# Optimization experiments

Hardware: AMD Instinct MI355X
Metric: run time of the kernel (lower is better)

## Reference

```python
import math
import jax, jax.numpy as jnp
import numpy as np

T, C, NH = 2048, 1024, 16
HD = C // NH


def setup_inputs() -> dict:
    key = jax.random.key(0)
    ks = jax.random.split(key, 5)
    return {
        "x": jax.random.normal(ks[0], (T, C), dtype=jnp.float32),
        "w_attn": jax.random.normal(ks[1], (3 * C, C), dtype=jnp.float32) * (1.0 / math.sqrt(C)),
        "b_attn": jax.random.normal(ks[2], (3 * C,), dtype=jnp.float32) * 0.02,
        "w_proj": jax.random.normal(ks[3], (C, C), dtype=jnp.float32) * (1.0 / math.sqrt(C)),
        "b_proj": jax.random.normal(ks[4], (C,), dtype=jnp.float32) * 0.02,
    }


def reference(x, w_attn, b_attn, w_proj, b_proj):
    t, c = x.shape
    # qkv projection: eqx Linear computes W @ x + b, vmapped over T
    qkv = x @ w_attn.T + b_attn  # (T, 3C)
    q, k, v = jnp.split(qkv, 3, axis=1)  # each (T, C)
    # (T, NH, HD) -> (NH, T, HD)
    q = jnp.swapaxes(q.reshape(t, NH, HD), 0, 1)
    k = jnp.swapaxes(k.reshape(t, NH, HD), 0, 1)
    v = jnp.swapaxes(v.reshape(t, NH, HD), 0, 1)
    att = jnp.einsum('hqd,hkd->hqk', q, k) / math.sqrt(HD)  # (NH, T, T)
    causal = jnp.tril(jnp.ones((t, t), dtype=bool))
    att = jnp.where(causal[None, :, :], att, -jnp.inf)
    att = jax.nn.softmax(att, axis=-1)
    y = jnp.matmul(att, v)  # (NH, T, HD)
    # Faithful to source: swapaxes(1,2) on (NH, T, HD) -> (NH, HD, T), then reshape
    y = jnp.swapaxes(y, 1, 2).reshape(t, c)
    return y @ w_proj.T + b_proj
```

## Files before the change

### kernel.cpp

```cpp
#include <hip/hip_runtime.h>
#include <hip/hip_bf16.h>
#include <stdint.h>

typedef __bf16 bf16;
typedef __bf16 bf16x8 __attribute__((ext_vector_type(8)));
typedef __bf16 bf16x4 __attribute__((ext_vector_type(4)));
typedef float floatx4 __attribute__((ext_vector_type(4)));

#define T_DIM 2048
#define C_DIM 1024
#define NH    16
#define HD    64

__device__ __forceinline__ void gload_lds16(const void* g, void* l) {
    __builtin_amdgcn_global_load_lds(
        (__attribute__((address_space(1))) void*)(g),
        (__attribute__((address_space(3))) void*)(l),
        16, 0, 0);
}

#define MFMA16(a, b, c) __builtin_amdgcn_mfma_f32_16x16x32_bf16(a, b, c, 0, 0, 0)

__global__ __launch_bounds__(256) void cvt_all(
    const float* __restrict__ x, const float* __restrict__ wa,
    const float* __restrict__ wp,
    bf16* __restrict__ xb, bf16* __restrict__ wab, bf16* __restrict__ wpb)
{
    const int i = blockIdx.x * 256 + threadIdx.x;
    const float* src; bf16* dst; int off;
    if (i < 262144)      { src = x;  dst = xb;  off = i; }
    else if (i < 655360) { src = wa; dst = wab; off = i - 262144; }
    else                 { src = wp; dst = wpb; off = i - 655360; }
    const float4 a = ((const float4*)src)[off * 2];
    const float4 b = ((const float4*)src)[off * 2 + 1];
    bf16x8 o;
    o[0] = (bf16)a.x; o[1] = (bf16)a.y; o[2] = (bf16)a.z; o[3] = (bf16)a.w;
    o[4] = (bf16)b.x; o[5] = (bf16)b.y; o[6] = (bf16)b.z; o[7] = (bf16)b.w;
    *(bf16x8*)(dst + (size_t)off * 8) = o;
}

template<int MODE, int TN>
__global__ __launch_bounds__(256) void csa_gemm_bt(
    const bf16* __restrict__ A, const bf16* __restrict__ B,
    const float* __restrict__ bias,
    void* __restrict__ out0v, bf16* __restrict__ out1, bf16* __restrict__ out2)
{
    constexpr int K = 1024;
    constexpr int MT = (TN == 128) ? 4 : 2;
    __shared__ __align__(16) bf16 sA[128 * 32];
    __shared__ __align__(16) bf16 sB[TN * 32];

    const int tid  = threadIdx.x;
    const int lane = tid & 63;
    const int wid  = tid >> 6;
    const int rowbase = (TN == 128) ? (wid & 1) * 64 : wid * 32;
    const int colbase = (TN == 128) ? (wid >> 1) * 64 : 0;
    const int tileM = blockIdx.x * 128;
    const int tileN = blockIdx.y * TN;

    const int r0 = tid >> 2;
    const int c0 = (tid & 3) * 8;
    const long aBase = (long)(tileM + r0) * K + c0;
    const long bBase = (long)(tileN + r0) * K + c0;

    const int fr   = lane & 15;
    const int quad = lane >> 4;
    const int fc   = quad * 8;

    floatx4 acc[MT][4];
#pragma unroll
    for (int i = 0; i < MT; i++)
#pragma unroll
        for (int j = 0; j < 4; j++) acc[i][j] = (floatx4){0.f, 0.f, 0.f, 0.f};

    for (int k0 = 0; k0 < K; k0 += 32) {
        __syncthreads();
        gload_lds16(A + aBase + k0,                 sA + tid * 8);
        gload_lds16(A + aBase + (long)64 * K + k0,  sA + 2048 + tid * 8);
        gload_lds16(B + bBase + k0,                 sB + tid * 8);
        if (TN == 128)
            gload_lds16(B + bBase + (long)64 * K + k0, sB + 2048 + tid * 8);
        __syncthreads();

        bf16x8 af[MT], bfr[4];
#pragma unroll
        for (int mt = 0; mt < MT; mt++)
            af[mt] = *(const bf16x8*)(sA + (rowbase + mt * 16 + fr) * 32 + fc);
#pragma unroll
        for (int nt = 0; nt < 4; nt++)
            bfr[nt] = *(const bf16x8*)(sB + (colbase + nt * 16 + fr) * 32 + fc);
#pragma unroll
        for (int mt = 0; mt < MT; mt++)
#pragma unroll
            for (int nt = 0; nt < 4; nt++)
                acc[mt][nt] = MFMA16(af[mt], bfr[nt], acc[mt][nt]);
    }

#pragma unroll
    for (int mt = 0; mt < MT; mt++) {
#pragma unroll
        for (int nt = 0; nt < 4; nt++) {
            const int gn = tileN + colbase + nt * 16 + fr;
            const float bv = bias[gn];
            const int gmb = tileM + rowbase + mt * 16 + quad * 4;
            if (MODE == 0) {
                const int which = gn >> 10;
                const int w2 = gn & 1023;
                const int hh = w2 >> 6, d = w2 & 63;
                if (which == 2) {
                    bf16x4 pk;
#pragma unroll
                    for (int r = 0; r < 4; r++) pk[r] = (bf16)(acc[mt][nt][r] + bv);
                    *(bf16x4*)(out2 + ((long)(hh * HD + d) << 11) + gmb) = pk;
                } else {
                    bf16* dst = (which == 0) ? (bf16*)out0v : out1;
#pragma unroll
                    for (int r = 0; r < 4; r++)
                        dst[((long)hh * T_DIM + gmb + r) * HD + d] =
                            (bf16)(acc[mt][nt][r] + bv);
                }
            } else {
#pragma unroll
                for (int r = 0; r < 4; r++)
                    ((float*)out0v)[(long)(gmb + r) * C_DIM + gn] =
                        acc[mt][nt][r] + bv;
            }
        }
    }
}

__global__ __launch_bounds__(256) void csa_attn_chunk(
    const bf16* __restrict__ Qh, const bf16* __restrict__ Kh,
    const bf16* __restrict__ Vth, float* __restrict__ Opart,
    float* __restrict__ lpart, bf16* __restrict__ YY)
{
    __shared__ __align__(16) bf16 sK[2][64 * 64];
    __shared__ __align__(16) bf16 sV[2][64 * 64];
    __shared__ __align__(16) bf16 sP[4][16 * 64];

    const int qt = blockIdx.x;
    const int h  = blockIdx.y;
    const int c  = blockIdx.z;
    const int nk = qt + 1;
    const int kt0 = c * 8;
    if (kt0 >= nk) return;
    const int ktend = (kt0 + 8 < nk) ? kt0 + 8 : nk;

    const int tid  = threadIdx.x;
    const int lane = tid & 63;
    const int wid  = tid >> 6;
    const int fr   = lane & 15;
    const int quad = lane >> 4;
    const int f7   = fr & 7;
    const int q0   = qt * 64;
    const int qg   = q0 + wid * 16 + fr;

    const bf16* qrow = Qh + ((long)h * T_DIM + qg) * HD;
    const bf16x8 qf0 = *(const bf16x8*)(qrow + quad * 8);
    const bf16x8 qf1 = *(const bf16x8*)(qrow + quad * 8 + 32);

    const int rb   = tid >> 3;
    const int cswz = (tid & 7) ^ (rb & 7);

    auto stage = [&](int b, int k0) {
        gload_lds16(Kh + ((long)(h * T_DIM + k0 + rb) << 6) + cswz * 8,
                    &sK[b][0] + tid * 8);
        gload_lds16(Kh + ((long)(h * T_DIM + k0 + rb + 32) << 6) + cswz * 8,
                    &sK[b][0] + 2048 + tid * 8);
        gload_lds16(Vth + ((long)(h * HD + rb) << 11) + k0 + cswz * 8,
                    &sV[b][0] + tid * 8);
        gload_lds16(Vth + ((long)(h * HD + rb + 32) << 11) + k0 + cswz * 8,
                    &sV[b][0] + 2048 + tid * 8);
    };

    stage(0, kt0 * 64);

    float l_i = 0.f;
    floatx4 o_acc[4];
#pragma unroll
    for (int d4 = 0; d4 < 4; d4++) o_acc[d4] = (floatx4){0.f, 0.f, 0.f, 0.f};

    for (int kt = kt0; kt < ktend; ++kt) {
        const int it = kt - kt0;
        __syncthreads();
        if (kt + 1 < ktend) stage((it + 1) & 1, (kt + 1) * 64);
        const bf16* K_ = &sK[it & 1][0];
        const bf16* V_ = &sV[it & 1][0];
        const int k0 = kt * 64;
        const bool diag = (kt == qt);

        float p[4][4];
#pragma unroll
        for (int nt = 0; nt < 4; nt++) {
            const bf16* kr = K_ + (nt * 16 + fr) * 64;
            const bf16x8 ka0 = *(const bf16x8*)(kr + (quad ^ f7) * 8);
            const bf16x8 ka1 = *(const bf16x8*)(kr + ((quad + 4) ^ f7) * 8);
            floatx4 z = (floatx4){0.f, 0.f, 0.f, 0.f};
            z = MFMA16(ka0, qf0, z);
            z = MFMA16(ka1, qf1, z);
            const int kgb = k0 + nt * 16 + quad * 4;
#pragma unroll
            for (int r = 0; r < 4; r++) {
                const float e = __builtin_amdgcn_exp2f(z[r] * 0.1803368801f);
                p[nt][r] = (!diag || (kgb + r <= qg)) ? e : 0.f;
            }
        }

        float s = 0.f;
#pragma unroll
        for (int nt = 0; nt < 4; nt++)
#pragma unroll
            for (int r = 0; r < 4; r++) s += p[nt][r];
        s += __shfl_xor(s, 16);
        s += __shfl_xor(s, 32);
        l_i += s;

        bf16* pw = &sP[wid][0];
#pragma unroll
        for (int nt = 0; nt < 4; nt++) {
            bf16x4 pk;
#pragma unroll
            for (int r = 0; r < 4; r++) pk[r] = (bf16)p[nt][r];
            *(bf16x4*)(pw + fr * 64 +
                       (((2 * nt + (quad >> 1)) ^ f7) * 8) + (quad & 1) * 4) = pk;
        }
        asm volatile("s_waitcnt lgkmcnt(0)" ::: "memory");
        const bf16x8 pa0 = *(const bf16x8*)(pw + fr * 64 + (quad ^ f7) * 8);
        const bf16x8 pa1 = *(const bf16x8*)(pw + fr * 64 + ((quad + 4) ^ f7) * 8);

#pragma unroll
        for (int d4 = 0; d4 < 4; d4++) {
            const bf16* vr = V_ + (d4 * 16 + fr) * 64;
            const bf16x8 vb0 = *(const bf16x8*)(vr + (quad ^ f7) * 8);
            const bf16x8 vb1 = *(const bf16x8*)(vr + ((quad + 4) ^ f7) * 8);
            o_acc[d4] = MFMA16(pa0, vb0, o_acc[d4]);
            o_acc[d4] = MFMA16(pa1, vb1, o_acc[d4]);
        }
    }

    if (kt0 == 0 && ktend == nk) {
        const float inv_self = 1.f / l_i;
        float inv[4];
#pragma unroll
        for (int r = 0; r < 4; r++) inv[r] = __shfl(inv_self, quad * 4 + r);
#pragma unroll
        for (int r = 0; r < 4; r++) {
            const int q = q0 + wid * 16 + quad * 4 + r;
            const int rq = q >> 10, cq = q & 1023;
#pragma unroll
            for (int d4 = 0; d4 < 4; d4++) {
                const int d = d4 * 16 + fr;
                YY[(long)(h * 128 + 2 * d + rq) * 1024 + cq] =
                    (bf16)(o_acc[d4][r] * inv[r]);
            }
        }
    } else {
        const long obase = ((long)((h * 32 + qt) * 4 + c)) * 4096;
#pragma unroll
        for (int d4 = 0; d4 < 4; d4++)
#pragma unroll
            for (int r = 0; r < 4; r++)
                Opart[obase + (wid * 16 + quad * 4 + r) * 64 + d4 * 16 + fr] =
                    o_acc[d4][r];
        if (quad == 0)
            lpart[((h * 32 + qt) * 4 + c) * 64 + wid * 16 + fr] = l_i;
    }
}

__global__ __launch_bounds__(256) void csa_combine(
    const float* __restrict__ Opart, const float* __restrict__ lpart,
    bf16* __restrict__ YY)
{
    const int qt = blockIdx.x + 8;
    const int h  = blockIdx.y;
    const int nc = (qt >> 3) + 1;
    const int t  = threadIdx.x;
    const int q  = t >> 2;
    const int d0 = (t & 3) * 16;

    const long obase = ((long)((h * 32 + qt) * 4)) * 4096 + q * 64 + d0;
    const int  lbase = (h * 32 + qt) * 4 * 64 + q;

    float4 acc[4] = {};
    float lq = 0.f;
    for (int c = 0; c < nc; c++) {
        const float4* src = (const float4*)(Opart + obase + (long)c * 4096);
#pragma unroll
        for (int j = 0; j < 4; j++) {
            const float4 v = src[j];
            acc[j].x += v.x; acc[j].y += v.y; acc[j].z += v.z; acc[j].w += v.w;
        }
        lq += lpart[lbase + c * 64];
    }
    const float inv = 1.f / lq;
    const int qglob = qt * 64 + q;
    const int rq = qglob >> 10, cq = qglob & 1023;
#pragma unroll
    for (int j = 0; j < 4; j++) {
        const float vv[4] = {acc[j].x, acc[j].y, acc[j].z, acc[j].w};
#pragma unroll
        for (int k = 0; k < 4; k++) {
            const int d = d0 + j * 4 + k;
            YY[(long)(h * 128 + 2 * d + rq) * 1024 + cq] = (bf16)(vv[k] * inv);
        }
    }
}

extern "C" void kernel_launch(void* const* d_in, const int* in_sizes, int n_in,
                              void* d_out, int out_size, void* d_ws, size_t ws_size,
                              hipStream_t stream) {
    (void)in_sizes; (void)n_in; (void)out_size; (void)ws_size;
    const float* x      = (const float*)d_in[0];
    const float* w_attn = (const float*)d_in[1];
    const float* b_attn = (const float*)d_in[2];
    const float* w_proj = (const float*)d_in[3];
    const float* b_proj = (const float*)d_in[4];

    bf16* xb  = (bf16*)d_ws;
    bf16* wab = xb  + (size_t)T_DIM * C_DIM;
    bf16* wpb = wab + (size_t)3 * C_DIM * C_DIM;
    bf16* Q   = wpb + (size_t)C_DIM * C_DIM;
    bf16* Kp  = Q   + (size_t)NH * T_DIM * HD;
    bf16* Vt  = Kp  + (size_t)NH * T_DIM * HD;
    bf16* YY  = Vt  + (size_t)NH * T_DIM * HD;
    float* Opart = (float*)(YY + (size_t)T_DIM * C_DIM);
    float* lpart = Opart + (size_t)16 * 32 * 4 * 4096;

    cvt_all<<<3072, 256, 0, stream>>>(x, w_attn, w_proj, xb, wab, wpb);

    csa_gemm_bt<0, 128><<<dim3(16, 24), 256, 0, stream>>>(xb, wab, b_attn, Q, Kp, Vt);
    csa_attn_chunk<<<dim3(32, NH, 4), 256, 0, stream>>>(Q, Kp, Vt, Opart, lpart, YY);
    csa_combine<<<dim3(24, NH), 256, 0, stream>>>(Opart, lpart, YY);
    csa_gemm_bt<1, 64><<<dim3(16, 16), 256, 0, stream>>>(YY, wpb, b_proj, d_out, nullptr, nullptr);
}
```

Measured before the change: 157.0 us.

## Enlarge attention query tile to 128 rows and launch heaviest tiles first

The attention kernel now gives each wave 32 query rows (two 16-row halves) instead of 16, so every K/V tile staged in shared memory serves twice as many queries. This halves K/V load traffic per query and doubles MFMA work per barrier. The grid is reordered so the longest causal query tiles are scheduled first, and the combine kernel and partial buffers are resized to match. The cost is higher register pressure, larger shared P buffers and fewer blocks, which can lower occupancy.

After: 162.0 us. 1.03x slower.

```diff
diff --git a/kernel.cpp b/kernel.cpp
--- a/kernel.cpp
+++ b/kernel.cpp
@@ -136,12 +136,12 @@
 {
     __shared__ __align__(16) bf16 sK[2][64 * 64];
     __shared__ __align__(16) bf16 sV[2][64 * 64];
-    __shared__ __align__(16) bf16 sP[4][16 * 64];
-
-    const int qt = blockIdx.x;
+    __shared__ __align__(16) bf16 sP[4][32 * 64];
+
+    const int c  = blockIdx.x;
     const int h  = blockIdx.y;
-    const int c  = blockIdx.z;
-    const int nk = qt + 1;
+    const int qt = 15 - (int)blockIdx.z;
+    const int nk = 2 * qt + 2;
     const int kt0 = c * 8;
     if (kt0 >= nk) return;
     const int ktend = (kt0 + 8 < nk) ? kt0 + 8 : nk;
@@ -152,12 +152,15 @@
     const int fr   = lane & 15;
     const int quad = lane >> 4;
     const int f7   = fr & 7;
-    const int q0   = qt * 64;
-    const int qg   = q0 + wid * 16 + fr;
-
-    const bf16* qrow = Qh + ((long)h * T_DIM + qg) * HD;
-    const bf16x8 qf0 = *(const bf16x8*)(qrow + quad * 8);
-    const bf16x8 qf1 = *(const bf16x8*)(qrow + quad * 8 + 32);
+    const int qw   = qt * 128 + wid * 32;
+
+    bf16x8 qf[2][2];
+#pragma unroll
+    for (int half = 0; half < 2; half++) {
+        const bf16* qrow = Qh + ((long)h * T_DIM + qw + half * 16 + fr) * HD;
+        qf[half][0] = *(const bf16x8*)(qrow + quad * 8);
+        qf[half][1] = *(const bf16x8*)(qrow + quad * 8 + 32);
+    }
 
     const int rb   = tid >> 3;
     const int cswz = (tid & 7) ^ (rb & 7);
@@ -175,10 +178,12 @@
 
     stage(0, kt0 * 64);
 
-    float l_i = 0.f;
-    floatx4 o_acc[4];
-#pragma unroll
-    for (int d4 = 0; d4 < 4; d4++) o_acc[d4] = (floatx4){0.f, 0.f, 0.f, 0.f};
+    float l_i[2] = {0.f, 0.f};
+    floatx4 o_acc[2][4];
+#pragma unroll
+    for (int half = 0; half < 2; half++)
+#pragma unroll
+        for (int d4 = 0; d4 < 4; d4++) o_acc[half][d4] = (floatx4){0.f, 0.f, 0.f, 0.f};
 
     for (int kt = kt0; kt < ktend; ++kt) {
         const int it = kt - kt0;
@@ -187,83 +192,108 @@
         const bf16* K_ = &sK[it & 1][0];
         const bf16* V_ = &sV[it & 1][0];
         const int k0 = kt * 64;
-        const bool diag = (kt == qt);
-
-        float p[4][4];
+        const bool need_mask = (kt >= 2 * qt);
+
+        float p[2][4][4];
 #pragma unroll
         for (int nt = 0; nt < 4; nt++) {
             const bf16* kr = K_ + (nt * 16 + fr) * 64;
             const bf16x8 ka0 = *(const bf16x8*)(kr + (quad ^ f7) * 8);
             const bf16x8 ka1 = *(const bf16x8*)(kr + ((quad + 4) ^ f7) * 8);
-            floatx4 z = (floatx4){0.f, 0.f, 0.f, 0.f};
-            z = MFMA16(ka0, qf0, z);
-            z = MFMA16(ka1, qf1, z);
             const int kgb = k0 + nt * 16 + quad * 4;
 #pragma unroll
-            for (int r = 0; r < 4; r++) {
-                const float e = __builtin_amdgcn_exp2f(z[r] * 0.1803368801f);
-                p[nt][r] = (!diag || (kgb + r <= qg)) ? e : 0.f;
-            }
-        }
-
-        float s = 0.f;
-#pragma unroll
-        for (int nt = 0; nt < 4; nt++)
-#pragma unroll
-            for (int r = 0; r < 4; r++) s += p[nt][r];
-        s += __shfl_xor(s, 16);
-        s += __shfl_xor(s, 32);
-        l_i += s;
+            for (int half = 0; half < 2; half++) {
+                floatx4 z = (floatx4){0.f, 0.f, 0.f, 0.f};
+                z = MFMA16(ka0, qf[half][0], z);
+                z = MFMA16(ka1, qf[half][1], z);
+                const int qg = qw + half * 16 + fr;
+#pragma unroll
+                for (int r = 0; r < 4; r++) {
+                    const float e = __builtin_amdgcn_exp2f(z[r] * 0.1803368801f);
+                    p[half][nt][r] = (!need_mask || (kgb + r <= qg)) ? e : 0.f;
+                }
+            }
+        }
+
+#pragma unroll
+        for (int half = 0; half < 2; half++) {
+            float s = 0.f;
+#pragma unroll
+            for (int nt = 0; nt < 4; nt++)
+#pragma unroll
+                for (int r = 0; r < 4; r++) s += p[half][nt][r];
+            s += __shfl_xor(s, 16);
+            s += __shfl_xor(s, 32);
+            l_i[half] += s;
+        }
 
         bf16* pw = &sP[wid][0];
 #pragma unroll
-        for (int nt = 0; nt < 4; nt++) {
-            bf16x4 pk;
-#pragma unroll
-            for (int r = 0; r < 4; r++) pk[r] = (bf16)p[nt][r];
-            *(bf16x4*)(pw + fr * 64 +
-                       (((2 * nt + (quad >> 1)) ^ f7) * 8) + (quad & 1) * 4) = pk;
-        }
+        for (int half = 0; half < 2; half++)
+#pragma unroll
+            for (int nt = 0; nt < 4; nt++) {
+                bf16x4 pk;
+#pragma unroll
+                for (int r = 0; r < 4; r++) pk[r] = (bf16)p[half][nt][r];
+                *(bf16x4*)(pw + (half * 16 + fr) * 64 +
+                           (((2 * nt + (quad >> 1)) ^ f7) * 8) + (quad & 1) * 4) = pk;
+            }
         asm volatile("s_waitcnt lgkmcnt(0)" ::: "memory");
-        const bf16x8 pa0 = *(const bf16x8*)(pw + fr * 64 + (quad ^ f7) * 8);
-        const bf16x8 pa1 = *(const bf16x8*)(pw + fr * 64 + ((quad + 4) ^ f7) * 8);
+        bf16x8 pa[2][2];
+#pragma unroll
+        for (int half = 0; half < 2; half++) {
+            pa[half][0] = *(const bf16x8*)(pw + (half * 16 + fr) * 64 + (quad ^ f7) * 8);
+            pa[half][1] = *(const bf16x8*)(pw + (half * 16 + fr) * 64 + ((quad + 4) ^ f7) * 8);
+        }
 
 #pragma unroll
         for (int d4 = 0; d4 < 4; d4++) {
             const bf16* vr = V_ + (d4 * 16 + fr) * 64;
             const bf16x8 vb0 = *(const bf16x8*)(vr + (quad ^ f7) * 8);
             const bf16x8 vb1 = *(const bf16x8*)(vr + ((quad + 4) ^ f7) * 8);
-            o_acc[d4] = MFMA16(pa0, vb0, o_acc[d4]);
-            o_acc[d4] = MFMA16(pa1, vb1, o_acc[d4]);
+#pragma unroll
+            for (int half = 0; half < 2; half++) {
+                o_acc[half][d4] = MFMA16(pa[half][0], vb0, o_acc[half][d4]);
+                o_acc[half][d4] = MFMA16(pa[half][1], vb1, o_acc[half][d4]);
+            }
         }
     }
 
     if (kt0 == 0 && ktend == nk) {
-        const float inv_self = 1.f / l_i;
-        float inv[4];
-#pragma unroll
-        for (int r = 0; r < 4; r++) inv[r] = __shfl(inv_self, quad * 4 + r);
-#pragma unroll
-        for (int r = 0; r < 4; r++) {
-            const int q = q0 + wid * 16 + quad * 4 + r;
-            const int rq = q >> 10, cq = q & 1023;
-#pragma unroll
-            for (int d4 = 0; d4 < 4; d4++) {
-                const int d = d4 * 16 + fr;
-                YY[(long)(h * 128 + 2 * d + rq) * 1024 + cq] =
-                    (bf16)(o_acc[d4][r] * inv[r]);
+#pragma unroll
+        for (int half = 0; half < 2; half++) {
+            const float inv_self = 1.f / l_i[half];
+            float inv[4];
+#pragma unroll
+            for (int r = 0; r < 4; r++) inv[r] = __shfl(inv_self, quad * 4 + r);
+#pragma unroll
+            for (int r = 0; r < 4; r++) {
+                const int q = qw + half * 16 + quad * 4 + r;
+                const int rq = q >> 10, cq = q & 1023;
+#pragma unroll
+                for (int d4 = 0; d4 < 4; d4++) {
+                    const int d = d4 * 16 + fr;
+                    YY[(long)(h * 128 + 2 * d + rq) * 1024 + cq] =
+                        (bf16)(o_acc[half][d4][r] * inv[r]);
+                }
             }
         }
     } else {
-        const long obase = ((long)((h * 32 + qt) * 4 + c)) * 4096;
-#pragma unroll
-        for (int d4 = 0; d4 < 4; d4++)
-#pragma unroll
-            for (int r = 0; r < 4; r++)
-                Opart[obase + (wid * 16 + quad * 4 + r) * 64 + d4 * 16 + fr] =
-                    o_acc[d4][r];
-        if (quad == 0)
-            lpart[((h * 32 + qt) * 4 + c) * 64 + wid * 16 + fr] = l_i;
+        const long obase = ((long)((h * 16 + qt) * 4 + c)) * 8192;
+#pragma unroll
+        for (int half = 0; half < 2; half++)
+#pragma unroll
+            for (int d4 = 0; d4 < 4; d4++)
+#pragma unroll
+                for (int r = 0; r < 4; r++)
+                    Opart[obase + (wid * 32 + half * 16 + quad * 4 + r) * 64 +
+                          d4 * 16 + fr] = o_acc[half][d4][r];
+        if (quad == 0) {
+#pragma unroll
+            for (int half = 0; half < 2; half++)
+                lpart[((h * 16 + qt) * 4 + c) * 128 + wid * 32 + half * 16 + fr] =
+                    l_i[half];
+        }
     }
 }
 
@@ -271,32 +301,32 @@
     const float* __restrict__ Opart, const float* __restrict__ lpart,
     bf16* __restrict__ YY)
 {
-    const int qt = blockIdx.x + 8;
+    const int qt = blockIdx.x + 4;
     const int h  = blockIdx.y;
-    const int nc = (qt >> 3) + 1;
+    const int nc = (2 * qt + 2 + 7) >> 3;
     const int t  = threadIdx.x;
-    const int q  = t >> 2;
-    const int d0 = (t & 3) * 16;
-
-    const long obase = ((long)((h * 32 + qt) * 4)) * 4096 + q * 64 + d0;
-    const int  lbase = (h * 32 + qt) * 4 * 64 + q;
-
-    float4 acc[4] = {};
+    const int row = t >> 1;
+    const int d0  = (t & 1) * 32;
+
+    const long obase = ((long)((h * 16 + qt) * 4)) * 8192 + row * 64 + d0;
+    const int  lbase = (h * 16 + qt) * 4 * 128 + row;
+
+    float4 acc[8] = {};
     float lq = 0.f;
     for (int c = 0; c < nc; c++) {
-        const float4* src = (const float4*)(Opart + obase + (long)c * 4096);
-#pragma unroll
-        for (int j = 0; j < 4; j++) {
+        const float4* src = (const float4*)(Opart + obase + (long)c * 8192);
+#pragma unroll
+        for (int j = 0; j < 8; j++) {
             const float4 v = src[j];
             acc[j].x += v.x; acc[j].y += v.y; acc[j].z += v.z; acc[j].w += v.w;
         }
-        lq += lpart[lbase + c * 64];
+        lq += lpart[lbase + c * 128];
     }
     const float inv = 1.f / lq;
-    const int qglob = qt * 64 + q;
+    const int qglob = qt * 128 + row;
     const int rq = qglob >> 10, cq = qglob & 1023;
 #pragma unroll
-    for (int j = 0; j < 4; j++) {
+    for (int j = 0; j < 8; j++) {
         const float vv[4] = {acc[j].x, acc[j].y, acc[j].z, acc[j].w};
 #pragma unroll
         for (int k = 0; k < 4; k++) {
@@ -324,12 +354,12 @@
     bf16* Vt  = Kp  + (size_t)NH * T_DIM * HD;
     bf16* YY  = Vt  + (size_t)NH * T_DIM * HD;
     float* Opart = (float*)(YY + (size_t)T_DIM * C_DIM);
-    float* lpart = Opart + (size_t)16 * 32 * 4 * 4096;
+    float* lpart = Opart + (size_t)16 * 16 * 4 * 8192;
 
     cvt_all<<<3072, 256, 0, stream>>>(x, w_attn, w_proj, xb, wab, wpb);
 
     csa_gemm_bt<0, 128><<<dim3(16, 24), 256, 0, stream>>>(xb, wab, b_attn, Q, Kp, Vt);
-    csa_attn_chunk<<<dim3(32, NH, 4), 256, 0, stream>>>(Q, Kp, Vt, Opart, lpart, YY);
-    csa_combine<<<dim3(24, NH), 256, 0, stream>>>(Opart, lpart, YY);
+    csa_attn_chunk<<<dim3(4, NH, 16), 256, 0, stream>>>(Q, Kp, Vt, Opart, lpart, YY);
+    csa_combine<<<dim3(12, NH), 256, 0, stream>>>(Opart, lpart, YY);
     csa_gemm_bt<1, 64><<<dim3(16, 16), 256, 0, stream>>>(YY, wpb, b_proj, d_out, nullptr, nullptr);
 }
```
